# Optimization experiments

Measured on AMD Instinct MI355X. Metric: run time of the kernel, lower is better.

## Reference

```python
import jax, jax.numpy as jnp
import numpy as np

B, S, I, H, A = 512, 256, 12, 256, 9


def _lstm_layer(x, w_ih, w_hh, b_ih, b_hh):
    # x: [B,S,in] -> outputs [B,S,H], final (h, c). PyTorch gate order i,f,g,o.
    b, s, _ = x.shape
    h_dim = w_hh.shape[1]
    xg = jnp.einsum('bsi,gi->bsg', x, w_ih) + b_ih  # [B,S,4H] precomputed input gates

    def step(carry, xg_t):
        h, c = carry
        gates = xg_t + h @ w_hh.T + b_hh
        i_g, f_g, g_g, o_g = jnp.split(gates, 4, axis=-1)
        c = jax.nn.sigmoid(f_g) * c + jax.nn.sigmoid(i_g) * jnp.tanh(g_g)
        h = jax.nn.sigmoid(o_g) * jnp.tanh(c)
        return (h, c), h

    init = (jnp.zeros((b, h_dim), x.dtype), jnp.zeros((b, h_dim), x.dtype))
    (h, c), ys = jax.lax.scan(step, init, jnp.swapaxes(xg, 0, 1))
    return jnp.swapaxes(ys, 0, 1), h, c


def setup_inputs() -> dict:
    key = jax.random.key(0)
    ks = jax.random.split(key, 20)
    sc = 0.1
    inp = {
        'x': jax.random.normal(ks[0], (B, S, I), jnp.float32),
        'mask': jnp.ones((B, A), jnp.float32),
        'W_emb': jax.random.normal(ks[1], (H, I), jnp.float32) * sc,
        'b_emb': jnp.zeros((H,), jnp.float32),
        'w_ih0': jax.random.normal(ks[2], (4 * H, H), jnp.float32) * sc,
        'w_hh0': jax.random.normal(ks[3], (4 * H, H), jnp.float32) * sc,
        'b_ih0': jnp.zeros((4 * H,), jnp.float32),
        'b_hh0': jnp.zeros((4 * H,), jnp.float32),
        'w_ih1': jax.random.normal(ks[4], (4 * H, H), jnp.float32) * sc,
        'w_hh1': jax.random.normal(ks[5], (4 * H, H), jnp.float32) * sc,
        'b_ih1': jnp.zeros((4 * H,), jnp.float32),
        'b_hh1': jnp.zeros((4 * H,), jnp.float32),
        'ln_g': jnp.ones((H,), jnp.float32),
        'ln_b': jnp.zeros((H,), jnp.float32),
        'w1': jax.random.normal(ks[6], (32, H), jnp.float32) * sc,
        'b1': jnp.zeros((32,), jnp.float32),
        'w2': jax.random.normal(ks[7], (A, 32), jnp.float32) * sc,
        'b2': jnp.zeros((A,), jnp.float32),
    }
    return inp


def reference(x, mask, W_emb, b_emb, w_ih0, w_hh0, b_ih0, b_hh0,
              w_ih1, w_hh1, b_ih1, b_hh1, ln_g, ln_b, w1, b1, w2, b2):
    # embed + ReLU
    emb = jax.nn.relu(jnp.einsum('bsi,hi->bsh', x, W_emb) + b_emb)  # [B,S,H]
    # 2-layer LSTM (dropout between layers is identity in eval mode)
    y0, h0, c0 = _lstm_layer(emb, w_ih0, w_hh0, b_ih0, b_hh0)
    y1, h1, c1 = _lstm_layer(y0, w_ih1, w_hh1, b_ih1, b_hh1)
    last = y1[:, -1, :]  # [B,H]
    # LayerNorm
    mu = jnp.mean(last, axis=-1, keepdims=True)
    var = jnp.mean((last - mu) ** 2, axis=-1, keepdims=True)
    normed = (last - mu) / jnp.sqrt(var + 1e-5) * ln_g + ln_b
    # MLP head (dropout identity in eval)
    hdn = jax.nn.relu(normed @ w1.T + b1)
    logits = hdn @ w2.T + b2  # [B,A]
    logits = logits + (1.0 - mask) * -1e9
    hidden = (jnp.stack([h0, h1]), jnp.stack([c0, c1]))
    return logits, hidden
```

## Files before the change

kernel.cpp:

```cpp
#include <hip/hip_runtime.h>
#include <cstdint>
#include <cstddef>

typedef __attribute__((ext_vector_type(8))) short short8;
typedef __attribute__((ext_vector_type(4))) float f32x4;

#define MFMA16(a, b, c) __builtin_amdgcn_mfma_f32_16x16x32_bf16((a), (b), (c), 0, 0, 0)
#define ALOAD64(p)   __hip_atomic_load((p), __ATOMIC_RELAXED, __HIP_MEMORY_SCOPE_AGENT)
#define ASTORE32(p, v) __hip_atomic_store((p), (v), __ATOMIC_RELAXED, __HIP_MEMORY_SCOPE_AGENT)

constexpr int kB = 512, kS = 256, kI = 12, kH = 256, kA = 9;
constexpr int kNS = 8;
constexpr int kNB = 32;
constexpr int kT  = 512;
constexpr int LDH = 264;
constexpr int LDG = 132;
constexpr int kBH = kB * kH;

constexpr int OUT_H = kB * kA;
constexpr int OUT_C = OUT_H + 2 * kBH;

__device__ __forceinline__ short f2bf(float f) {
  uint32_t u = __float_as_uint(f);
  u += 0x7fffu + ((u >> 16) & 1u);
  return (short)(u >> 16);
}
__device__ __forceinline__ float fast_sigmoid(float v) {
  return __builtin_amdgcn_rcpf(1.f + __expf(-v));
}
__device__ __forceinline__ float fast_tanh(float v) {
  return 2.f * __builtin_amdgcn_rcpf(1.f + __expf(-2.f * v)) - 1.f;
}

__global__ __launch_bounds__(kT, 2) void lstm_scan_kernel(
    const float* __restrict__ x,
    const float* __restrict__ W_emb, const float* __restrict__ b_emb,
    const float* __restrict__ w_ih0, const float* __restrict__ w_hh0,
    const float* __restrict__ b_ih0, const float* __restrict__ b_hh0,
    const float* __restrict__ w_ih1, const float* __restrict__ w_hh1,
    const float* __restrict__ b_ih1, const float* __restrict__ b_hh1,
    uint32_t* __restrict__ h0ex, uint32_t* __restrict__ h1ex,
    float* __restrict__ dout)
{
  const int tid   = threadIdx.x;
  const int btile = blockIdx.x & (kNB - 1);
  const int slice = blockIdx.x >> 5;
  const int b0    = btile * 16;
  const int lane  = tid & 63;
  const int wave  = tid >> 6;
  const int n16   = lane & 15;
  const int quad  = lane >> 4;

  __shared__ short embL[16 * LDH];
  __shared__ short hA[16 * LDH];
  __shared__ short hB[16 * LDH];
  __shared__ float gL0[16 * LDG];
  __shared__ float gL1[16 * LDG];

  for (int i = tid; i < 16 * LDH; i += kT) { hA[i] = 0; hB[i] = 0; }

  const float* Wm[4] = { w_ih0, w_hh0, w_ih1, w_hh1 };
  short8 wB[4][8];
  {
    const int gcol = (wave >> 1) * kH + slice * 32 + (wave & 1) * 16 + n16;
#pragma unroll
    for (int mat = 0; mat < 4; ++mat) {
      const float* wp = Wm[mat] + (size_t)gcol * kH;
#pragma unroll
      for (int kk = 0; kk < 8; ++kk) {
        const float* p = wp + kk * 32 + quad * 8;
        const float4 f0 = *(const float4*)p;
        const float4 f1 = *(const float4*)(p + 4);
        short8 v;
        v[0] = f2bf(f0.x); v[1] = f2bf(f0.y); v[2] = f2bf(f0.z); v[3] = f2bf(f0.w);
        v[4] = f2bf(f1.x); v[5] = f2bf(f1.y); v[6] = f2bf(f1.z); v[7] = f2bf(f1.w);
        wB[mat][kk] = v;
      }
    }
  }
  short8 wE[2];
  float bembv[2];
#pragma unroll
  for (int i = 0; i < 2; ++i) {
    const int col = wave * 32 + i * 16 + n16;
    short8 v;
#pragma unroll
    for (int j = 0; j < 8; ++j) {
      const int k = quad * 8 + j;
      v[j] = (k < kI) ? f2bf(W_emb[col * kI + k]) : (short)0;
    }
    wE[i] = v;
    bembv[i] = b_emb[col];
  }
  const int erow = tid >> 5;
  const int ec   = tid & 31;
  const int ecol = slice * 32 + ec;
  float bi0[4], bi1[4];
#pragma unroll
  for (int g = 0; g < 4; ++g) {
    bi0[g] = b_ih0[g * kH + ecol] + b_hh0[g * kH + ecol];
    bi1[g] = b_ih1[g * kH + ecol] + b_hh1[g * kH + ecol];
  }
  float c0v = 0.f, c1v = 0.f;

  {
    const float* xr = x + (size_t)(b0 + n16) * kS * kI;
    short8 xa;
#pragma unroll
    for (int j = 0; j < 8; ++j) {
      const int k = quad * 8 + j;
      xa[j] = (k < kI) ? f2bf(xr[k]) : (short)0;
    }
#pragma unroll
    for (int i = 0; i < 2; ++i) {
      f32x4 z = {0.f, 0.f, 0.f, 0.f};
      f32x4 e = MFMA16(xa, wE[i], z);
      const int col = wave * 32 + i * 16 + n16;
#pragma unroll
      for (int r = 0; r < 4; ++r) {
        float v = e[r] + bembv[i];
        v = v > 0.f ? v : 0.f;
        embL[(quad * 4 + r) * LDH + col] = f2bf(v);
      }
    }
  }
  __syncthreads();

  for (int p = 0; p <= kS; ++p) {
    const int par = p & 1;
    const uint32_t tag = (uint32_t)((p + 1) & 255);

    {
      f32x4 a0 = {0.f,0.f,0.f,0.f}, g1 = a0;
#pragma unroll
      for (int kk = 0; kk < 8; ++kk) {
        const short8 ha = *(const short8*)&hA[n16 * LDH + kk * 32 + quad * 8];
        a0 = MFMA16(ha, wB[1][kk], a0);
        g1 = MFMA16(ha, wB[2][kk], g1);
      }
#pragma unroll
      for (int kk = 0; kk < 8; ++kk) {
        const short8 e = *(const short8*)&embL[n16 * LDH + kk * 32 + quad * 8];
        a0 = MFMA16(e, wB[0][kk], a0);
      }
#pragma unroll
      for (int kk = 0; kk < 8; ++kk) {
        const short8 hb = *(const short8*)&hB[n16 * LDH + kk * 32 + quad * 8];
        g1 = MFMA16(hb, wB[3][kk], g1);
      }
      const int lcol = (wave >> 1) * 32 + (wave & 1) * 16 + n16;
#pragma unroll
      for (int r = 0; r < 4; ++r) {
        gL0[(quad * 4 + r) * LDG + lcol] = a0[r];
        gL1[(quad * 4 + r) * LDG + lcol] = g1[r];
      }
    }
    __syncthreads();

    if (p < kS) {
      const float iv = gL0[erow * LDG +       ec] + bi0[0];
      const float fv = gL0[erow * LDG +  32 + ec] + bi0[1];
      const float gv = gL0[erow * LDG +  64 + ec] + bi0[2];
      const float ov = gL0[erow * LDG +  96 + ec] + bi0[3];
      const float c = fast_sigmoid(fv) * c0v + fast_sigmoid(iv) * fast_tanh(gv);
      c0v = c;
      const float h = fast_sigmoid(ov) * fast_tanh(c);
      const uint32_t pk = ((uint32_t)(uint16_t)f2bf(h) << 16) | tag;
      ASTORE32(&h0ex[(size_t)par * kBH + (size_t)(b0 + erow) * kH + ecol], pk);
      if (p == kS - 1) {
        dout[OUT_H + (size_t)(b0 + erow) * kH + ecol] = h;
        dout[OUT_C + (size_t)(b0 + erow) * kH + ecol] = c;
      }
    }
    {
      float h = 0.f;
      if (p >= 1) {
        const float iv = gL1[erow * LDG +       ec] + bi1[0];
        const float fv = gL1[erow * LDG +  32 + ec] + bi1[1];
        const float gv = gL1[erow * LDG +  64 + ec] + bi1[2];
        const float ov = gL1[erow * LDG +  96 + ec] + bi1[3];
        const float c = fast_sigmoid(fv) * c1v + fast_sigmoid(iv) * fast_tanh(gv);
        c1v = c;
        h = fast_sigmoid(ov) * fast_tanh(c);
      }
      const uint32_t pk = ((uint32_t)(uint16_t)f2bf(h) << 16) | tag;
      ASTORE32(&h1ex[(size_t)par * kBH + (size_t)(b0 + erow) * kH + ecol], pk);
      if (p == kS) {
        dout[OUT_H + kBH + (size_t)(b0 + erow) * kH + ecol] = h;
        dout[OUT_C + kBH + (size_t)(b0 + erow) * kH + ecol] = c1v;
      }
    }

    if (p < kS) {
      if (p + 1 < kS) {
        const float* xr = x + ((size_t)(b0 + n16) * kS + (p + 1)) * kI;
        short8 xa;
#pragma unroll
        for (int j = 0; j < 8; ++j) {
          const int k = quad * 8 + j;
          xa[j] = (k < kI) ? f2bf(xr[k]) : (short)0;
        }
#pragma unroll
        for (int i = 0; i < 2; ++i) {
          f32x4 z = {0.f, 0.f, 0.f, 0.f};
          f32x4 e = MFMA16(xa, wE[i], z);
          const int col = wave * 32 + i * 16 + n16;
#pragma unroll
          for (int r = 0; r < 4; ++r) {
            float v = e[r] + bembv[i];
            v = v > 0.f ? v : 0.f;
            embL[(quad * 4 + r) * LDH + col] = f2bf(v);
          }
        }
      }

      {
        const int rr = tid >> 5;
        const int cu = tid & 31;
        const size_t base = (size_t)par * kBH + (size_t)(b0 + rr) * kH;
        const uint64_t* s0 = (const uint64_t*)&h0ex[base];
        const uint64_t* s1 = (const uint64_t*)&h1ex[base];
        uint64_t v0[4], v1[4];
        for (;;) {
          bool ok = true;
#pragma unroll
          for (int k = 0; k < 4; ++k) v0[k] = ALOAD64(s0 + cu + 32 * k);
#pragma unroll
          for (int k = 0; k < 4; ++k) v1[k] = ALOAD64(s1 + cu + 32 * k);
#pragma unroll
          for (int k = 0; k < 4; ++k) {
            ok = ok & (((uint32_t)v0[k] & 255u) == tag) & (((uint32_t)(v0[k] >> 32) & 255u) == tag);
            ok = ok & (((uint32_t)v1[k] & 255u) == tag) & (((uint32_t)(v1[k] >> 32) & 255u) == tag);
          }
          if (ok) break;
          __builtin_amdgcn_s_sleep(1);
        }
#pragma unroll
        for (int k = 0; k < 4; ++k) {
          const int c2 = cu * 2 + 64 * k;
          hA[rr * LDH + c2]     = (short)((uint32_t)v0[k] >> 16);
          hA[rr * LDH + c2 + 1] = (short)(v0[k] >> 48);
          hB[rr * LDH + c2]     = (short)((uint32_t)v1[k] >> 16);
          hB[rr * LDH + c2 + 1] = (short)(v1[k] >> 48);
        }
      }
      __syncthreads();
    }
  }
}

__global__ __launch_bounds__(64) void head_kernel(
    const float* __restrict__ h1last, const float* __restrict__ mask,
    const float* __restrict__ ln_g, const float* __restrict__ ln_b,
    const float* __restrict__ w1, const float* __restrict__ b1,
    const float* __restrict__ w2, const float* __restrict__ b2,
    float* __restrict__ out)
{
  const int r = blockIdx.x;
  const int lane = threadIdx.x;
  __shared__ float ns[kH];
  __shared__ float hd[32];
  const float4 v = *(const float4*)&h1last[r * kH + lane * 4];
  float vv[4] = {v.x, v.y, v.z, v.w};
  float s = vv[0] + vv[1] + vv[2] + vv[3];
#pragma unroll
  for (int off = 32; off > 0; off >>= 1) s += __shfl_xor(s, off, 64);
  const float mean = s * (1.f / kH);
  float q = 0.f;
#pragma unroll
  for (int j = 0; j < 4; ++j) { const float d = vv[j] - mean; q += d * d; }
#pragma unroll
  for (int off = 32; off > 0; off >>= 1) q += __shfl_xor(q, off, 64);
  const float rstd = rsqrtf(q * (1.f / kH) + 1e-5f);
#pragma unroll
  for (int j = 0; j < 4; ++j) {
    const int c = lane * 4 + j;
    ns[c] = (vv[j] - mean) * rstd * ln_g[c] + ln_b[c];
  }
  __syncthreads();
  if (lane < 32) {
    float a = b1[lane];
    const float* wr = w1 + lane * kH;
    for (int k = 0; k < kH; ++k) a += ns[k] * wr[k];
    hd[lane] = a > 0.f ? a : 0.f;
  }
  __syncthreads();
  if (lane < kA) {
    float a = b2[lane];
    const float* wr = w2 + lane * 32;
#pragma unroll
    for (int k = 0; k < 32; ++k) a += hd[k] * wr[k];
    a += (1.f - mask[r * kA + lane]) * (-1e9f);
    out[r * kA + lane] = a;
  }
}

extern "C" void kernel_launch(void* const* d_in, const int* in_sizes, int n_in,
                              void* d_out, int out_size, void* d_ws, size_t ws_size,
                              hipStream_t stream)
{
  (void)in_sizes; (void)n_in; (void)out_size; (void)ws_size;
  const float* x     = (const float*)d_in[0];
  const float* mask  = (const float*)d_in[1];
  const float* W_emb = (const float*)d_in[2];
  const float* b_emb = (const float*)d_in[3];
  const float* w_ih0 = (const float*)d_in[4];
  const float* w_hh0 = (const float*)d_in[5];
  const float* b_ih0 = (const float*)d_in[6];
  const float* b_hh0 = (const float*)d_in[7];
  const float* w_ih1 = (const float*)d_in[8];
  const float* w_hh1 = (const float*)d_in[9];
  const float* b_ih1 = (const float*)d_in[10];
  const float* b_hh1 = (const float*)d_in[11];
  const float* ln_g  = (const float*)d_in[12];
  const float* ln_b  = (const float*)d_in[13];
  const float* w1    = (const float*)d_in[14];
  const float* b1    = (const float*)d_in[15];
  const float* w2    = (const float*)d_in[16];
  const float* b2    = (const float*)d_in[17];
  float* out = (float*)d_out;

  uint32_t* h0ex = (uint32_t*)d_ws;
  uint32_t* h1ex = h0ex + 2 * kBH;

  lstm_scan_kernel<<<dim3(kNB * kNS), dim3(kT), 0, stream>>>(
      x, W_emb, b_emb, w_ih0, w_hh0, b_ih0, b_hh0, w_ih1, w_hh1, b_ih1, b_hh1,
      h0ex, h1ex, out);

  head_kernel<<<dim3(kB), dim3(64), 0, stream>>>(
      out + OUT_H + kBH, mask, ln_g, ln_b, w1, b1, w2, b2, out);
}
```

Baseline: 1.056 ms.

## Split layer-1 recurrence into two phases to overlap cross-block h exchange

Restructures the persistent two-layer LSTM loop so the layer-0 and layer-1 hidden-state exchanges wait separately. The layer-1 h poll is deferred and overlapped with the layer-0 hA matmul and the next embedding computation. Layer-1 gates are then finished in a second phase, so its h for the current step is published within the same iteration. Spin-wait loads are also reorganised per thread with packed 32-bit LDS writes. This adds two extra block barriers per step in exchange for shortening the critical path of the cross-block dependency chain.

```diff
diff --git a/kernel.cpp b/kernel.cpp
--- a/kernel.cpp
+++ b/kernel.cpp
@@ -126,34 +126,26 @@
   }
   __syncthreads();
 
+  const int lcol = (wave >> 1) * 32 + (wave & 1) * 16 + n16;
+
   for (int p = 0; p <= kS; ++p) {
     const int par = p & 1;
-    const uint32_t tag = (uint32_t)((p + 1) & 255);
-
-    {
-      f32x4 a0 = {0.f,0.f,0.f,0.f}, g1 = a0;
+    const uint32_t tagh0 = (uint32_t)((p + 1) & 255);
+
+    if (p < kS) {
+      f32x4 a0 = {0.f, 0.f, 0.f, 0.f};
+#pragma unroll
+      for (int kk = 0; kk < 8; ++kk) {
+        const short8 e = *(const short8*)&embL[n16 * LDH + kk * 32 + quad * 8];
+        a0 = MFMA16(e, wB[0][kk], a0);
+      }
 #pragma unroll
       for (int kk = 0; kk < 8; ++kk) {
         const short8 ha = *(const short8*)&hA[n16 * LDH + kk * 32 + quad * 8];
         a0 = MFMA16(ha, wB[1][kk], a0);
-        g1 = MFMA16(ha, wB[2][kk], g1);
-      }
-#pragma unroll
-      for (int kk = 0; kk < 8; ++kk) {
-        const short8 e = *(const short8*)&embL[n16 * LDH + kk * 32 + quad * 8];
-        a0 = MFMA16(e, wB[0][kk], a0);
-      }
-#pragma unroll
-      for (int kk = 0; kk < 8; ++kk) {
-        const short8 hb = *(const short8*)&hB[n16 * LDH + kk * 32 + quad * 8];
-        g1 = MFMA16(hb, wB[3][kk], g1);
-      }
-      const int lcol = (wave >> 1) * 32 + (wave & 1) * 16 + n16;
-#pragma unroll
-      for (int r = 0; r < 4; ++r) {
-        gL0[(quad * 4 + r) * LDG + lcol] = a0[r];
-        gL1[(quad * 4 + r) * LDG + lcol] = g1[r];
-      }
+      }
+#pragma unroll
+      for (int r = 0; r < 4; ++r) gL0[(quad * 4 + r) * LDG + lcol] = a0[r];
     }
     __syncthreads();
 
@@ -165,87 +157,108 @@
       const float c = fast_sigmoid(fv) * c0v + fast_sigmoid(iv) * fast_tanh(gv);
       c0v = c;
       const float h = fast_sigmoid(ov) * fast_tanh(c);
-      const uint32_t pk = ((uint32_t)(uint16_t)f2bf(h) << 16) | tag;
+      const uint32_t pk = ((uint32_t)(uint16_t)f2bf(h) << 16) | tagh0;
       ASTORE32(&h0ex[(size_t)par * kBH + (size_t)(b0 + erow) * kH + ecol], pk);
       if (p == kS - 1) {
         dout[OUT_H + (size_t)(b0 + erow) * kH + ecol] = h;
         dout[OUT_C + (size_t)(b0 + erow) * kH + ecol] = c;
       }
     }
+    if (p >= 2) {
+      const uint32_t tg = (uint32_t)((p - 1) & 255);
+      const uint64_t* s = (const uint64_t*)&h1ex[(size_t)par * kBH + (size_t)(b0 + erow) * kH];
+      uint64_t v[4];
+      for (;;) {
+        bool ok = true;
+#pragma unroll
+        for (int k = 0; k < 4; ++k) v[k] = ALOAD64(s + ec + 32 * k);
+#pragma unroll
+        for (int k = 0; k < 4; ++k)
+          ok = ok & (((uint32_t)v[k] & 255u) == tg) & (((uint32_t)(v[k] >> 32) & 255u) == tg);
+        if (ok) break;
+        __builtin_amdgcn_s_sleep(1);
+      }
+#pragma unroll
+      for (int k = 0; k < 4; ++k) {
+        const uint32_t two = ((uint32_t)(v[k] >> 16) & 0xFFFFu) | ((uint32_t)(v[k] >> 48) << 16);
+        *(uint32_t*)&hB[erow * LDH + ec * 2 + 64 * k] = two;
+      }
+    }
+    f32x4 g1 = {0.f, 0.f, 0.f, 0.f};
+#pragma unroll
+    for (int kk = 0; kk < 8; ++kk) {
+      const short8 ha = *(const short8*)&hA[n16 * LDH + kk * 32 + quad * 8];
+      g1 = MFMA16(ha, wB[2][kk], g1);
+    }
+    if (p + 1 < kS) {
+      const float* xr = x + ((size_t)(b0 + n16) * kS + (p + 1)) * kI;
+      short8 xa;
+#pragma unroll
+      for (int j = 0; j < 8; ++j) {
+        const int k = quad * 8 + j;
+        xa[j] = (k < kI) ? f2bf(xr[k]) : (short)0;
+      }
+#pragma unroll
+      for (int i = 0; i < 2; ++i) {
+        f32x4 z = {0.f, 0.f, 0.f, 0.f};
+        f32x4 e = MFMA16(xa, wE[i], z);
+        const int col = wave * 32 + i * 16 + n16;
+#pragma unroll
+        for (int r = 0; r < 4; ++r) {
+          float v = e[r] + bembv[i];
+          v = v > 0.f ? v : 0.f;
+          embL[(quad * 4 + r) * LDH + col] = f2bf(v);
+        }
+      }
+    }
+    __syncthreads();
+
     {
-      float h = 0.f;
-      if (p >= 1) {
-        const float iv = gL1[erow * LDG +       ec] + bi1[0];
-        const float fv = gL1[erow * LDG +  32 + ec] + bi1[1];
-        const float gv = gL1[erow * LDG +  64 + ec] + bi1[2];
-        const float ov = gL1[erow * LDG +  96 + ec] + bi1[3];
-        const float c = fast_sigmoid(fv) * c1v + fast_sigmoid(iv) * fast_tanh(gv);
-        c1v = c;
-        h = fast_sigmoid(ov) * fast_tanh(c);
-      }
-      const uint32_t pk = ((uint32_t)(uint16_t)f2bf(h) << 16) | tag;
-      ASTORE32(&h1ex[(size_t)par * kBH + (size_t)(b0 + erow) * kH + ecol], pk);
+#pragma unroll
+      for (int kk = 0; kk < 8; ++kk) {
+        const short8 hb = *(const short8*)&hB[n16 * LDH + kk * 32 + quad * 8];
+        g1 = MFMA16(hb, wB[3][kk], g1);
+      }
+#pragma unroll
+      for (int r = 0; r < 4; ++r) gL1[(quad * 4 + r) * LDG + lcol] = g1[r];
+    }
+    __syncthreads();
+
+    if (p >= 1) {
+      const float iv = gL1[erow * LDG +       ec] + bi1[0];
+      const float fv = gL1[erow * LDG +  32 + ec] + bi1[1];
+      const float gv = gL1[erow * LDG +  64 + ec] + bi1[2];
+      const float ov = gL1[erow * LDG +  96 + ec] + bi1[3];
+      const float c = fast_sigmoid(fv) * c1v + fast_sigmoid(iv) * fast_tanh(gv);
+      c1v = c;
+      const float h = fast_sigmoid(ov) * fast_tanh(c);
+      const uint32_t pk = ((uint32_t)(uint16_t)f2bf(h) << 16) | (uint32_t)(p & 255);
+      ASTORE32(&h1ex[(size_t)((p - 1) & 1) * kBH + (size_t)(b0 + erow) * kH + ecol], pk);
       if (p == kS) {
         dout[OUT_H + kBH + (size_t)(b0 + erow) * kH + ecol] = h;
-        dout[OUT_C + kBH + (size_t)(b0 + erow) * kH + ecol] = c1v;
-      }
-    }
-
+        dout[OUT_C + kBH + (size_t)(b0 + erow) * kH + ecol] = c;
+      }
+    }
     if (p < kS) {
-      if (p + 1 < kS) {
-        const float* xr = x + ((size_t)(b0 + n16) * kS + (p + 1)) * kI;
-        short8 xa;
-#pragma unroll
-        for (int j = 0; j < 8; ++j) {
-          const int k = quad * 8 + j;
-          xa[j] = (k < kI) ? f2bf(xr[k]) : (short)0;
-        }
-#pragma unroll
-        for (int i = 0; i < 2; ++i) {
-          f32x4 z = {0.f, 0.f, 0.f, 0.f};
-          f32x4 e = MFMA16(xa, wE[i], z);
-          const int col = wave * 32 + i * 16 + n16;
-#pragma unroll
-          for (int r = 0; r < 4; ++r) {
-            float v = e[r] + bembv[i];
-            v = v > 0.f ? v : 0.f;
-            embL[(quad * 4 + r) * LDH + col] = f2bf(v);
-          }
-        }
-      }
-
-      {
-        const int rr = tid >> 5;
-        const int cu = tid & 31;
-        const size_t base = (size_t)par * kBH + (size_t)(b0 + rr) * kH;
-        const uint64_t* s0 = (const uint64_t*)&h0ex[base];
-        const uint64_t* s1 = (const uint64_t*)&h1ex[base];
-        uint64_t v0[4], v1[4];
-        for (;;) {
-          bool ok = true;
-#pragma unroll
-          for (int k = 0; k < 4; ++k) v0[k] = ALOAD64(s0 + cu + 32 * k);
-#pragma unroll
-          for (int k = 0; k < 4; ++k) v1[k] = ALOAD64(s1 + cu + 32 * k);
-#pragma unroll
-          for (int k = 0; k < 4; ++k) {
-            ok = ok & (((uint32_t)v0[k] & 255u) == tag) & (((uint32_t)(v0[k] >> 32) & 255u) == tag);
-            ok = ok & (((uint32_t)v1[k] & 255u) == tag) & (((uint32_t)(v1[k] >> 32) & 255u) == tag);
-          }
-          if (ok) break;
-          __builtin_amdgcn_s_sleep(1);
-        }
-#pragma unroll
-        for (int k = 0; k < 4; ++k) {
-          const int c2 = cu * 2 + 64 * k;
-          hA[rr * LDH + c2]     = (short)((uint32_t)v0[k] >> 16);
-          hA[rr * LDH + c2 + 1] = (short)(v0[k] >> 48);
-          hB[rr * LDH + c2]     = (short)((uint32_t)v1[k] >> 16);
-          hB[rr * LDH + c2 + 1] = (short)(v1[k] >> 48);
-        }
-      }
-      __syncthreads();
-    }
+      const uint64_t* s = (const uint64_t*)&h0ex[(size_t)par * kBH + (size_t)(b0 + erow) * kH];
+      uint64_t v[4];
+      for (;;) {
+        bool ok = true;
+#pragma unroll
+        for (int k = 0; k < 4; ++k) v[k] = ALOAD64(s + ec + 32 * k);
+#pragma unroll
+        for (int k = 0; k < 4; ++k)
+          ok = ok & (((uint32_t)v[k] & 255u) == tagh0) & (((uint32_t)(v[k] >> 32) & 255u) == tagh0);
+        if (ok) break;
+        __builtin_amdgcn_s_sleep(1);
+      }
+#pragma unroll
+      for (int k = 0; k < 4; ++k) {
+        const uint32_t two = ((uint32_t)(v[k] >> 16) & 0xFFFFu) | ((uint32_t)(v[k] >> 48) << 16);
+        *(uint32_t*)&hA[erow * LDH + ec * 2 + 64 * k] = two;
+      }
+    }
+    __syncthreads();
   }
 }
 
```

Measured after the change: 1.064 ms. About the same (+0.8%).
